# Kernel tuning notes

Hardware: AMD Instinct MI355X
Metric: run time of the kernel (lower is better)

Reference implementation:

```python
import jax, jax.numpy as jnp
import numpy as np

NUM_CLASS = 22  # restypes_with_x_and_gap: 20 AAs + 'X' + '-' (gap is last)


def layer_norm(x, g, b, eps=1e-5):
    mu = jnp.mean(x, axis=-1, keepdims=True)
    var = jnp.var(x, axis=-1, keepdims=True)
    return (x - mu) * jax.lax.rsqrt(var + eps) * g + b


def setup_inputs() -> dict:
    key = jax.random.key(0)
    ks = jax.random.split(key, 8)
    B, M, N, DS, DP = 1, 128, 256, 384, 128
    C = NUM_CLASS
    s = 0.02
    return dict(
        single=jax.random.normal(ks[0], (B, N, DS), dtype=jnp.float32),
        pair=jax.random.normal(ks[1], (B, N, N, DP), dtype=jnp.float32),
        msa=jax.random.randint(ks[2], (B, M, N), 0, C),
        w1=jax.random.normal(ks[3], (DS, DS), dtype=jnp.float32) * s,
        b1=jnp.zeros((DS,), jnp.float32),
        g1=jnp.ones((DS,), jnp.float32),
        be1=jnp.zeros((DS,), jnp.float32),
        w2=jax.random.normal(ks[4], (DS, C), dtype=jnp.float32) * s,
        b2=jnp.zeros((C,), jnp.float32),
        g2=jnp.ones((DP,), jnp.float32),
        be2=jnp.zeros((DP,), jnp.float32),
        w3=jax.random.normal(ks[5], (DP, C * C), dtype=jnp.float32) * s,
        b3=jnp.zeros((C * C,), jnp.float32),
    )


def reference(single, pair, msa, w1, b1, g1, be1, w2, b2, g2, be2, w3, b3):
    C = NUM_CLASS
    B, N = single.shape[0], single.shape[1]
    # make_mask(restypes_with_x_and_gap, '-'): 1 everywhere except the gap class (last index)
    label_mask = jnp.ones((C,), single.dtype).at[C - 1].set(0.0)

    # single branch: Linear -> GELU(exact) -> LayerNorm -> Linear
    h = jax.nn.gelu(single @ w1 + b1, approximate=False)
    ei = layer_norm(h, g1, be1) @ w2 + b2  # [B, N, C]

    # pairwise branch: symmetrize -> LayerNorm -> Linear -> ReLU, zero diagonal
    zsym = (pair + jnp.swapaxes(pair, 1, 2)) * 0.5
    eij = jax.nn.relu(layer_norm(zsym, g2, be2) @ w3 + b3)  # [B, N, N, C*C]
    eij = eij * (1.0 - jnp.eye(N, dtype=eij.dtype))[:, :, None]

    # coevolution logits: one-hot MSA (with gap class masked) contracted with pairwise couplings
    eijcd = eij.reshape(B, N, N, C, C)
    oh = jax.nn.one_hot(msa, C, dtype=eij.dtype) * label_mask  # [B, M, N, C] fold mask 'd' into one-hot
    hi = jnp.einsum('bmjd,bijcd->bmic', oh, eijcd)  # [B, M, N, C]
    logits = ei[:, None] + hi  # [B, M, N, C]
    return eij, ei, logits
```

## Files before the change

### kernel.cpp

```cpp
#include <hip/hip_runtime.h>
#include <hip/hip_bf16.h>

#define NN 256
#define MM 128
#define DS 384
#define DP 128
#define CC 22
#define C2 484

#define OUT_EI  (NN*NN*C2)
#define OUT_LOG (OUT_EI + NN*CC)

typedef __attribute__((ext_vector_type(8))) short short8;
typedef __attribute__((ext_vector_type(4))) float f32x4;

__device__ __forceinline__ unsigned f2bf(float x) {
  unsigned u = __float_as_uint(x);
  return (u + 0x7FFFu + ((u >> 16) & 1u)) >> 16;
}

__global__ void k_w3pack(const float* __restrict__ w3, int4* __restrict__ w3f) {
  int ct = blockIdx.x, kt = blockIdx.y, l = threadIdx.x;
  int c = ct * 16 + (l & 15);
  int kb = kt * 32 + (l >> 4) * 8;
  unsigned v[8];
#pragma unroll
  for (int e = 0; e < 8; ++e) {
    float x = (c < C2) ? w3[(kb + e) * C2 + c] : 0.f;
    v[e] = f2bf(x);
  }
  int4 pk;
  pk.x = (int)(v[0] | (v[1] << 16));
  pk.y = (int)(v[2] | (v[3] << 16));
  pk.z = (int)(v[4] | (v[5] << 16));
  pk.w = (int)(v[6] | (v[7] << 16));
  w3f[(kt * 31 + ct) * 64 + l] = pk;
}

extern "C" __global__ __launch_bounds__(512) void k_fused(
    const float* __restrict__ single, const float* __restrict__ pair,
    const int* __restrict__ msa,
    const float* __restrict__ w1, const float* __restrict__ b1,
    const float* __restrict__ g1, const float* __restrict__ be1,
    const float* __restrict__ w2, const float* __restrict__ b2,
    const float* __restrict__ g2, const float* __restrict__ be2,
    const float* __restrict__ b3, const int4* __restrict__ w3f,
    float* __restrict__ outp)
{
  extern __shared__ char smem[];
  float* out_eij = outp;
  float* out_ei  = outp + OUT_EI;
  float* out_log = outp + OUT_LOG;

  const int i = blockIdx.x;
  const int t = threadIdx.x;
  const int w = t >> 6, l = t & 63;
  const int lr = l & 15, lg = l >> 4;

  float* srow = (float*)smem;
  float* hlx  = (float*)(smem + 1536);
  float* part = (float*)(smem + 3072);
  float* wred = (float*)(smem + 4480);
  float* wredq= (float*)(smem + 4512);
  float* mur  = (float*)(smem + 4544);

  if (t < DS) srow[t] = single[i * DS + t];
  __syncthreads();
  float hv = 0.f;
  if (t < DS) {
    float acc = b1[t];
#pragma unroll 8
    for (int d = 0; d < DS; ++d) acc = fmaf(srow[d], w1[d * DS + t], acc);
    hv = 0.5f * acc * (1.0f + erff(acc * 0.70710678118654752f));
    float s = hv, q = hv * hv;
#pragma unroll
    for (int off = 32; off; off >>= 1) { s += __shfl_xor(s, off); q += __shfl_xor(q, off); }
    if ((t & 63) == 0) { wred[t >> 6] = s; wredq[t >> 6] = q; }
  }
  __syncthreads();
  if (t == 0) {
    float S = 0.f, Q = 0.f;
    for (int ww = 0; ww < 6; ++ww) { S += wred[ww]; Q += wredq[ww]; }
    float mu = S / (float)DS;
    mur[0] = mu; mur[1] = rsqrtf(Q / (float)DS - mu * mu + 1e-5f);
  }
  __syncthreads();
  if (t < DS) hlx[t] = (hv - mur[0]) * mur[1] * g1[t] + be1[t];
  __syncthreads();
  if (t < 352) {
    int g = t / 22, c = t - g * 22;
    float p = 0.f;
#pragma unroll
    for (int k = g * 24; k < g * 24 + 24; ++k) p = fmaf(hlx[k], w2[k * CC + c], p);
    part[t] = p;
  }
  __syncthreads();
  if (t < CC) {
    float sm = b2[t];
#pragma unroll
    for (int g = 0; g < 16; ++g) sm += part[g * CC + t];
    out_ei[i * CC + t] = sm;
  }
  __syncthreads();

  {
    float2 g2v = ((const float2*)g2)[l];
    float2 bev = ((const float2*)be2)[l];
    for (int it = 0; it < 32; ++it) {
      int j = w * 32 + it;
      float2 a = ((const float2*)(pair + (i * NN + j) * DP))[l];
      float2 b = ((const float2*)(pair + (j * NN + i) * DP))[l];
      float zx = 0.5f * (a.x + b.x), zy = 0.5f * (a.y + b.y);
      float s = zx + zy, q = zx * zx + zy * zy;
#pragma unroll
      for (int off = 32; off; off >>= 1) { s += __shfl_xor(s, off); q += __shfl_xor(q, off); }
      float mu = s * (1.f / 128.f);
      float rs = rsqrtf(q * (1.f / 128.f) - mu * mu + 1e-5f);
      float nx = (zx - mu) * rs * g2v.x + bev.x;
      float ny = (zy - mu) * rs * g2v.y + bev.y;
      unsigned pk = f2bf(nx) | (f2bf(ny) << 16);
      int blk = (l >> 2) ^ (j & 15);
      *(unsigned*)(smem + j * 256 + blk * 16 + (l & 3) * 4) = pk;
    }
  }
  __syncthreads();

  {
    int jt0 = 2 * w, jt1 = 2 * w + 1;
    short8 a0[4], a1[4];
#pragma unroll
    for (int kt = 0; kt < 4; ++kt) {
      int blk = kt * 4 + lg;
      int j0 = jt0 * 16 + lr;
      int j1 = jt1 * 16 + lr;
      a0[kt] = *(const short8*)(smem + j0 * 256 + (blk ^ (j0 & 15)) * 16);
      a1[kt] = *(const short8*)(smem + j1 * 256 + (blk ^ (j1 & 15)) * 16);
    }
    const short8* w3fv = (const short8*)w3f;
    for (int ct = 0; ct < 31; ++ct) {
      f32x4 acc0 = {0.f, 0.f, 0.f, 0.f}, acc1 = {0.f, 0.f, 0.f, 0.f};
#pragma unroll
      for (int kt = 0; kt < 4; ++kt) {
        short8 bfr = w3fv[(kt * 31 + ct) * 64 + l];
        acc0 = __builtin_amdgcn_mfma_f32_16x16x32_bf16(a0[kt], bfr, acc0, 0, 0, 0);
        acc1 = __builtin_amdgcn_mfma_f32_16x16x32_bf16(a1[kt], bfr, acc1, 0, 0, 0);
      }
      int cflat = ct * 16 + lr;
      if (cflat < C2) {
        float bias = b3[cflat];
#pragma unroll
        for (int r = 0; r < 4; ++r) {
          int j0r = jt0 * 16 + lg * 4 + r;
          float v0 = fmaxf(acc0[r] + bias, 0.f);
          if (j0r == i) v0 = 0.f;
          out_eij[(i * NN + j0r) * C2 + cflat] = v0;
          int j1r = jt1 * 16 + lg * 4 + r;
          float v1 = fmaxf(acc1[r] + bias, 0.f);
          if (j1r == i) v1 = 0.f;
          out_eij[(i * NN + j1r) * C2 + cflat] = v1;
        }
      }
    }
  }
  __threadfence_block();
  __syncthreads();

  int* msa_s = (int*)(smem + 28672);
  for (int idx = t; idx < 28672 / 4; idx += 512) ((unsigned*)smem)[idx] = 0u;
  __syncthreads();

  f32x4 acc[2][2];
#pragma unroll
  for (int a_ = 0; a_ < 2; ++a_)
#pragma unroll
    for (int b_ = 0; b_ < 2; ++b_) acc[a_][b_] = (f32x4){0.f, 0.f, 0.f, 0.f};

  for (int jc = 0; jc < 16; ++jc) {
    {
      int m = t >> 2, qq = t & 3;
      int4 mv = *(const int4*)(msa + m * NN + jc * 16 + qq * 4);
      msa_s[(qq * 4 + 0) * 128 + m] = mv.x;
      msa_s[(qq * 4 + 1) * 128 + m] = mv.y;
      msa_s[(qq * 4 + 2) * 128 + m] = mv.z;
      msa_s[(qq * 4 + 3) * 128 + m] = mv.w;
    }
    for (int idx = t; idx < 1936; idx += 512) {
      int jj = idx / 121, p = idx - jj * 121;
      float4 v = ((const float4*)(out_eij + (i * NN + jc * 16 + jj) * C2))[p];
      float vv[4] = {v.x, v.y, v.z, v.w};
      int base = 4 * p;
#pragma unroll
      for (int q = 0; q < 4; ++q) {
        int fl = base + q;
        int c = fl / 22, d = fl - c * 22;
        *(unsigned short*)(smem + jj * 1584 + c * 72 + d * 2) = (unsigned short)f2bf(vv[q]);
      }
    }
    __syncthreads();
    if (w < 4) {
#pragma unroll 2
      for (int jj = 0; jj < 16; ++jj) {
#pragma unroll
        for (int cp = 0; cp < 2; ++cp) {
          short8 af = *(const short8*)(smem + jj * 1584 + (cp * 16 + lr) * 72 + lg * 16);
#pragma unroll
          for (int mti = 0; mti < 2; ++mti) {
            int s = msa_s[jj * 128 + (w * 2 + mti) * 16 + lr];
            int rel = s - lg * 8;
            unsigned hval = (s != 21 && ((unsigned)rel) < 8u) ? (0x3F80u << ((rel & 1) << 4)) : 0u;
            int word = rel >> 1;
            union { short8 s8; unsigned u[4]; } bu;
            bu.u[0] = (word == 0) ? hval : 0u;
            bu.u[1] = (word == 1) ? hval : 0u;
            bu.u[2] = (word == 2) ? hval : 0u;
            bu.u[3] = (word == 3) ? hval : 0u;
            acc[mti][cp] = __builtin_amdgcn_mfma_f32_16x16x32_bf16(af, bu.s8, acc[mti][cp], 0, 0, 0);
          }
        }
      }
    }
    __syncthreads();
  }

  if (w < 4) {
#pragma unroll
    for (int mti = 0; mti < 2; ++mti) {
      int m = (w * 2 + mti) * 16 + lr;
#pragma unroll
      for (int cp = 0; cp < 2; ++cp) {
#pragma unroll
        for (int r = 0; r < 4; ++r) {
          int c = cp * 16 + lg * 4 + r;
          if (c < CC) {
            out_log[(m * NN + i) * CC + c] = acc[mti][cp][r] + out_ei[i * CC + c];
          }
        }
      }
    }
  }
}

extern "C" void kernel_launch(void* const* d_in, const int* in_sizes, int n_in,
                              void* d_out, int out_size, void* d_ws, size_t ws_size,
                              hipStream_t stream) {
  const float* single = (const float*)d_in[0];
  const float* pairp  = (const float*)d_in[1];
  const int*   msa    = (const int*)d_in[2];
  const float* w1  = (const float*)d_in[3];
  const float* b1  = (const float*)d_in[4];
  const float* g1  = (const float*)d_in[5];
  const float* be1 = (const float*)d_in[6];
  const float* w2  = (const float*)d_in[7];
  const float* b2  = (const float*)d_in[8];
  const float* g2  = (const float*)d_in[9];
  const float* be2 = (const float*)d_in[10];
  const float* w3  = (const float*)d_in[11];
  const float* b3  = (const float*)d_in[12];

  int4* w3f = (int4*)d_ws;

  hipLaunchKernelGGL(k_w3pack, dim3(31, 4), dim3(64), 0, stream, w3, w3f);
  hipLaunchKernelGGL(k_fused, dim3(256), dim3(512), 65536, stream,
                     single, pairp, msa, w1, b1, g1, be1, w2, b2, g2, be2,
                     b3, (const int4*)w3f, (float*)d_out);
}
```

Baseline: 331.6 us.

## Split fused kernel: separate single-branch, split j across 2 blocks, in-LDS eij reuse

Moves the single-sequence MLP into its own kernel and pre-transposes the MSA to bytes. The main kernel now runs 512 blocks, with each block handling half of the j range. Within a block, j is processed in chunks of 32, and the bf16 eij tile is written directly into LDS instead of being re-read from global memory. Logits are accumulated with atomicAdd across the two j-halves into a buffer that k_single zeroes first. This raises parallelism and removes the global round-trip of eij, at the cost of atomics, extra launches and a dependence on kernel ordering.

```diff
diff --git a/kernel.cpp b/kernel.cpp
--- a/kernel.cpp
+++ b/kernel.cpp
@@ -37,77 +37,98 @@
   w3f[(kt * 31 + ct) * 64 + l] = pk;
 }
 
-extern "C" __global__ __launch_bounds__(512) void k_fused(
-    const float* __restrict__ single, const float* __restrict__ pair,
-    const int* __restrict__ msa,
-    const float* __restrict__ w1, const float* __restrict__ b1,
-    const float* __restrict__ g1, const float* __restrict__ be1,
-    const float* __restrict__ w2, const float* __restrict__ b2,
+__global__ void k_msat(const int* __restrict__ msa, unsigned char* __restrict__ mt) {
+  int j = blockIdx.x, m = threadIdx.x;
+  mt[j * MM + m] = (unsigned char)msa[m * NN + j];
+}
+
+__global__ __launch_bounds__(384) void k_single(
+    const float* __restrict__ single, const float* __restrict__ w1,
+    const float* __restrict__ b1, const float* __restrict__ g1,
+    const float* __restrict__ be1, const float* __restrict__ w2,
+    const float* __restrict__ b2, float* __restrict__ out_ei,
+    float* __restrict__ out_log)
+{
+  __shared__ float srow[DS];
+  __shared__ float hlx[DS];
+  __shared__ float part[16 * CC];
+  __shared__ float wred[8], wredq[8], mur[2];
+  int n = blockIdx.x, t = threadIdx.x;
+  srow[t] = single[n * DS + t];
+  for (int idx = t; idx < MM * CC; idx += 384) {
+    int m = idx / CC, c = idx - m * CC;
+    out_log[(m * NN + n) * CC + c] = 0.f;
+  }
+  __syncthreads();
+  float acc = b1[t];
+#pragma unroll 8
+  for (int d = 0; d < DS; ++d) acc = fmaf(srow[d], w1[d * DS + t], acc);
+  float hv = 0.5f * acc * (1.0f + erff(acc * 0.70710678118654752f));
+  float s = hv, q = hv * hv;
+#pragma unroll
+  for (int off = 32; off; off >>= 1) { s += __shfl_xor(s, off); q += __shfl_xor(q, off); }
+  if ((t & 63) == 0) { wred[t >> 6] = s; wredq[t >> 6] = q; }
+  __syncthreads();
+  if (t == 0) {
+    float S = 0.f, Q = 0.f;
+    for (int w = 0; w < 6; ++w) { S += wred[w]; Q += wredq[w]; }
+    float mu = S / (float)DS;
+    mur[0] = mu; mur[1] = rsqrtf(Q / (float)DS - mu * mu + 1e-5f);
+  }
+  __syncthreads();
+  hlx[t] = (hv - mur[0]) * mur[1] * g1[t] + be1[t];
+  __syncthreads();
+  if (t < 352) {
+    int g = t / CC, c = t - g * CC;
+    float p = 0.f;
+#pragma unroll
+    for (int k = g * 24; k < g * 24 + 24; ++k) p = fmaf(hlx[k], w2[k * CC + c], p);
+    part[t] = p;
+  }
+  __syncthreads();
+  if (t < CC) {
+    float sm = b2[t];
+#pragma unroll
+    for (int g = 0; g < 16; ++g) sm += part[g * CC + t];
+    out_ei[n * CC + t] = sm;
+  }
+}
+
+__global__ __launch_bounds__(512, 4) void k_fused(
+    const float* __restrict__ pair, const unsigned char* __restrict__ msa_tb,
     const float* __restrict__ g2, const float* __restrict__ be2,
     const float* __restrict__ b3, const int4* __restrict__ w3f,
-    float* __restrict__ outp)
+    const float* __restrict__ ei,
+    float* __restrict__ out_eij, float* __restrict__ out_log)
 {
-  extern __shared__ char smem[];
-  float* out_eij = outp;
-  float* out_ei  = outp + OUT_EI;
-  float* out_log = outp + OUT_LOG;
-
-  const int i = blockIdx.x;
+  __shared__ __align__(16) char smem[64512];
+  unsigned char* msa_s = (unsigned char*)(smem + 52224);
+  char* zln = smem + 56320;
+
+  const int i = blockIdx.x, jh = blockIdx.y;
   const int t = threadIdx.x;
   const int w = t >> 6, l = t & 63;
   const int lr = l & 15, lg = l >> 4;
 
-  float* srow = (float*)smem;
-  float* hlx  = (float*)(smem + 1536);
-  float* part = (float*)(smem + 3072);
-  float* wred = (float*)(smem + 4480);
-  float* wredq= (float*)(smem + 4512);
-  float* mur  = (float*)(smem + 4544);
-
-  if (t < DS) srow[t] = single[i * DS + t];
-  __syncthreads();
-  float hv = 0.f;
-  if (t < DS) {
-    float acc = b1[t];
-#pragma unroll 8
-    for (int d = 0; d < DS; ++d) acc = fmaf(srow[d], w1[d * DS + t], acc);
-    hv = 0.5f * acc * (1.0f + erff(acc * 0.70710678118654752f));
-    float s = hv, q = hv * hv;
-#pragma unroll
-    for (int off = 32; off; off >>= 1) { s += __shfl_xor(s, off); q += __shfl_xor(q, off); }
-    if ((t & 63) == 0) { wred[t >> 6] = s; wredq[t >> 6] = q; }
-  }
-  __syncthreads();
-  if (t == 0) {
-    float S = 0.f, Q = 0.f;
-    for (int ww = 0; ww < 6; ++ww) { S += wred[ww]; Q += wredq[ww]; }
-    float mu = S / (float)DS;
-    mur[0] = mu; mur[1] = rsqrtf(Q / (float)DS - mu * mu + 1e-5f);
-  }
-  __syncthreads();
-  if (t < DS) hlx[t] = (hv - mur[0]) * mur[1] * g1[t] + be1[t];
-  __syncthreads();
-  if (t < 352) {
-    int g = t / 22, c = t - g * 22;
-    float p = 0.f;
-#pragma unroll
-    for (int k = g * 24; k < g * 24 + 24; ++k) p = fmaf(hlx[k], w2[k * CC + c], p);
-    part[t] = p;
-  }
-  __syncthreads();
-  if (t < CC) {
-    float sm = b2[t];
-#pragma unroll
-    for (int g = 0; g < 16; ++g) sm += part[g * CC + t];
-    out_ei[i * CC + t] = sm;
-  }
-  __syncthreads();
-
-  {
-    float2 g2v = ((const float2*)g2)[l];
-    float2 bev = ((const float2*)be2)[l];
-    for (int it = 0; it < 32; ++it) {
-      int j = w * 32 + it;
+  for (int idx = t; idx < 52224 / 4; idx += 512) ((unsigned*)smem)[idx] = 0u;
+
+  f32x4 acc[2];
+  acc[0] = (f32x4){0.f, 0.f, 0.f, 0.f};
+  acc[1] = (f32x4){0.f, 0.f, 0.f, 0.f};
+
+  const float2 g2v = ((const float2*)g2)[l];
+  const float2 bev = ((const float2*)be2)[l];
+  const short8* w3fv = (const short8*)w3f;
+
+  __syncthreads();
+
+  for (int ch = 0; ch < 4; ++ch) {
+    const int j0 = jh * 128 + ch * 32;
+
+#pragma unroll
+    for (int it = 0; it < 4; ++it) {
+      int jl = w * 4 + it;
+      int j = j0 + jl;
       float2 a = ((const float2*)(pair + (i * NN + j) * DP))[l];
       float2 b = ((const float2*)(pair + (j * NN + i) * DP))[l];
       float zx = 0.5f * (a.x + b.x), zy = 0.5f * (a.y + b.y);
@@ -119,121 +140,80 @@
       float nx = (zx - mu) * rs * g2v.x + bev.x;
       float ny = (zy - mu) * rs * g2v.y + bev.y;
       unsigned pk = f2bf(nx) | (f2bf(ny) << 16);
-      int blk = (l >> 2) ^ (j & 15);
-      *(unsigned*)(smem + j * 256 + blk * 16 + (l & 3) * 4) = pk;
-    }
-  }
-  __syncthreads();
-
-  {
-    int jt0 = 2 * w, jt1 = 2 * w + 1;
+      int blk = (l >> 2) ^ (jl & 15);
+      *(unsigned*)(zln + jl * 256 + blk * 16 + (l & 3) * 4) = pk;
+    }
+    ((uint2*)msa_s)[t] = ((const uint2*)(msa_tb + j0 * MM))[t];
+    __syncthreads();
+
     short8 a0[4], a1[4];
 #pragma unroll
     for (int kt = 0; kt < 4; ++kt) {
-      int blk = kt * 4 + lg;
-      int j0 = jt0 * 16 + lr;
-      int j1 = jt1 * 16 + lr;
-      a0[kt] = *(const short8*)(smem + j0 * 256 + (blk ^ (j0 & 15)) * 16);
-      a1[kt] = *(const short8*)(smem + j1 * 256 + (blk ^ (j1 & 15)) * 16);
-    }
-    const short8* w3fv = (const short8*)w3f;
-    for (int ct = 0; ct < 31; ++ct) {
-      f32x4 acc0 = {0.f, 0.f, 0.f, 0.f}, acc1 = {0.f, 0.f, 0.f, 0.f};
+      a0[kt] = *(const short8*)(zln + lr * 256 + (((kt * 4 + lg) ^ lr) * 16));
+      a1[kt] = *(const short8*)(zln + (16 + lr) * 256 + (((kt * 4 + lg) ^ lr) * 16));
+    }
+    for (int ct = w; ct < 31; ct += 8) {
+      f32x4 c0 = {0.f, 0.f, 0.f, 0.f}, c1 = {0.f, 0.f, 0.f, 0.f};
 #pragma unroll
       for (int kt = 0; kt < 4; ++kt) {
         short8 bfr = w3fv[(kt * 31 + ct) * 64 + l];
-        acc0 = __builtin_amdgcn_mfma_f32_16x16x32_bf16(a0[kt], bfr, acc0, 0, 0, 0);
-        acc1 = __builtin_amdgcn_mfma_f32_16x16x32_bf16(a1[kt], bfr, acc1, 0, 0, 0);
+        c0 = __builtin_amdgcn_mfma_f32_16x16x32_bf16(a0[kt], bfr, c0, 0, 0, 0);
+        c1 = __builtin_amdgcn_mfma_f32_16x16x32_bf16(a1[kt], bfr, c1, 0, 0, 0);
       }
       int cflat = ct * 16 + lr;
       if (cflat < C2) {
         float bias = b3[cflat];
+        int cdiv = cflat / CC;
+        int dd = cflat - cdiv * CC;
 #pragma unroll
         for (int r = 0; r < 4; ++r) {
-          int j0r = jt0 * 16 + lg * 4 + r;
-          float v0 = fmaxf(acc0[r] + bias, 0.f);
-          if (j0r == i) v0 = 0.f;
-          out_eij[(i * NN + j0r) * C2 + cflat] = v0;
-          int j1r = jt1 * 16 + lg * 4 + r;
-          float v1 = fmaxf(acc1[r] + bias, 0.f);
-          if (j1r == i) v1 = 0.f;
-          out_eij[(i * NN + j1r) * C2 + cflat] = v1;
+          int jjl0 = lg * 4 + r;
+          int j = j0 + jjl0;
+          float v = fmaxf(c0[r] + bias, 0.f);
+          if (j == i) v = 0.f;
+          out_eij[(i * NN + j) * C2 + cflat] = v;
+          *(unsigned short*)(smem + jjl0 * 1584 + cdiv * 72 + dd * 2) = (unsigned short)f2bf(v);
+
+          int jjl1 = 16 + lg * 4 + r;
+          j = j0 + jjl1;
+          v = fmaxf(c1[r] + bias, 0.f);
+          if (j == i) v = 0.f;
+          out_eij[(i * NN + j) * C2 + cflat] = v;
+          *(unsigned short*)(smem + jjl1 * 1584 + cdiv * 72 + dd * 2) = (unsigned short)f2bf(v);
         }
       }
     }
-  }
-  __threadfence_block();
-  __syncthreads();
-
-  int* msa_s = (int*)(smem + 28672);
-  for (int idx = t; idx < 28672 / 4; idx += 512) ((unsigned*)smem)[idx] = 0u;
-  __syncthreads();
-
-  f32x4 acc[2][2];
-#pragma unroll
-  for (int a_ = 0; a_ < 2; ++a_)
-#pragma unroll
-    for (int b_ = 0; b_ < 2; ++b_) acc[a_][b_] = (f32x4){0.f, 0.f, 0.f, 0.f};
-
-  for (int jc = 0; jc < 16; ++jc) {
-    {
-      int m = t >> 2, qq = t & 3;
-      int4 mv = *(const int4*)(msa + m * NN + jc * 16 + qq * 4);
-      msa_s[(qq * 4 + 0) * 128 + m] = mv.x;
-      msa_s[(qq * 4 + 1) * 128 + m] = mv.y;
-      msa_s[(qq * 4 + 2) * 128 + m] = mv.z;
-      msa_s[(qq * 4 + 3) * 128 + m] = mv.w;
-    }
-    for (int idx = t; idx < 1936; idx += 512) {
-      int jj = idx / 121, p = idx - jj * 121;
-      float4 v = ((const float4*)(out_eij + (i * NN + jc * 16 + jj) * C2))[p];
-      float vv[4] = {v.x, v.y, v.z, v.w};
-      int base = 4 * p;
-#pragma unroll
-      for (int q = 0; q < 4; ++q) {
-        int fl = base + q;
-        int c = fl / 22, d = fl - c * 22;
-        *(unsigned short*)(smem + jj * 1584 + c * 72 + d * 2) = (unsigned short)f2bf(vv[q]);
-      }
-    }
     __syncthreads();
-    if (w < 4) {
-#pragma unroll 2
-      for (int jj = 0; jj < 16; ++jj) {
-#pragma unroll
-        for (int cp = 0; cp < 2; ++cp) {
-          short8 af = *(const short8*)(smem + jj * 1584 + (cp * 16 + lr) * 72 + lg * 16);
-#pragma unroll
-          for (int mti = 0; mti < 2; ++mti) {
-            int s = msa_s[jj * 128 + (w * 2 + mti) * 16 + lr];
-            int rel = s - lg * 8;
-            unsigned hval = (s != 21 && ((unsigned)rel) < 8u) ? (0x3F80u << ((rel & 1) << 4)) : 0u;
-            int word = rel >> 1;
-            union { short8 s8; unsigned u[4]; } bu;
-            bu.u[0] = (word == 0) ? hval : 0u;
-            bu.u[1] = (word == 1) ? hval : 0u;
-            bu.u[2] = (word == 2) ? hval : 0u;
-            bu.u[3] = (word == 3) ? hval : 0u;
-            acc[mti][cp] = __builtin_amdgcn_mfma_f32_16x16x32_bf16(af, bu.s8, acc[mti][cp], 0, 0, 0);
-          }
-        }
+
+    for (int jj = 0; jj < 32; ++jj) {
+      int s = msa_s[jj * 128 + w * 16 + lr];
+      int rel = s - lg * 8;
+      unsigned hval = (s != 21 && ((unsigned)rel) < 8u) ? (0x3F80u << ((rel & 1) << 4)) : 0u;
+      int word = rel >> 1;
+      union { short8 s8; unsigned u[4]; } bu;
+      bu.u[0] = (word == 0) ? hval : 0u;
+      bu.u[1] = (word == 1) ? hval : 0u;
+      bu.u[2] = (word == 2) ? hval : 0u;
+      bu.u[3] = (word == 3) ? hval : 0u;
+#pragma unroll
+      for (int cp = 0; cp < 2; ++cp) {
+        short8 af = *(const short8*)(smem + jj * 1584 + (cp * 16 + lr) * 72 + lg * 16);
+        acc[cp] = __builtin_amdgcn_mfma_f32_16x16x32_bf16(af, bu.s8, acc[cp], 0, 0, 0);
       }
     }
     __syncthreads();
   }
 
-  if (w < 4) {
-#pragma unroll
-    for (int mti = 0; mti < 2; ++mti) {
-      int m = (w * 2 + mti) * 16 + lr;
-#pragma unroll
-      for (int cp = 0; cp < 2; ++cp) {
-#pragma unroll
-        for (int r = 0; r < 4; ++r) {
-          int c = cp * 16 + lg * 4 + r;
-          if (c < CC) {
-            out_log[(m * NN + i) * CC + c] = acc[mti][cp][r] + out_ei[i * CC + c];
-          }
+  {
+    int m = w * 16 + lr;
+#pragma unroll
+    for (int cp = 0; cp < 2; ++cp) {
+#pragma unroll
+      for (int r = 0; r < 4; ++r) {
+        int c = cp * 16 + lg * 4 + r;
+        if (c < CC) {
+          float add = acc[cp][r] + (jh == 0 ? ei[i * CC + c] : 0.f);
+          atomicAdd(&out_log[(m * NN + i) * CC + c], add);
         }
       }
     }
@@ -257,10 +237,19 @@
   const float* w3  = (const float*)d_in[11];
   const float* b3  = (const float*)d_in[12];
 
+  float* out = (float*)d_out;
+  float* out_eij = out;
+  float* out_ei  = out + OUT_EI;
+  float* out_log = out + OUT_LOG;
+
   int4* w3f = (int4*)d_ws;
+  unsigned char* msa_tb = (unsigned char*)d_ws + 131072;
 
   hipLaunchKernelGGL(k_w3pack, dim3(31, 4), dim3(64), 0, stream, w3, w3f);
-  hipLaunchKernelGGL(k_fused, dim3(256), dim3(512), 65536, stream,
-                     single, pairp, msa, w1, b1, g1, be1, w2, b2, g2, be2,
-                     b3, (const int4*)w3f, (float*)d_out);
-}
+  hipLaunchKernelGGL(k_msat, dim3(NN), dim3(MM), 0, stream, msa, msa_tb);
+  hipLaunchKernelGGL(k_single, dim3(NN), dim3(384), 0, stream,
+                     single, w1, b1, g1, be1, w2, b2, out_ei, out_log);
+  hipLaunchKernelGGL(k_fused, dim3(256, 2), dim3(512), 0, stream,
+                     pairp, msa_tb, g2, be2, b3, (const int4*)w3f,
+                     out_ei, out_eij, out_log);
+}
```

After: 273.8 us. -17.4%, faster.
